# Optimization experiments

Hardware: AMD Instinct MI355X
Metric: run time of the kernel (lower is better)

The kernel has to match this reference:

```python
import jax, jax.numpy as jnp
import numpy as np

T, B, I, H, NC = 1024, 256, 128, 64, 10


def _lstm_cell(x_t, h, c, W_ih, W_hh, b):
    # PyTorch gate order: i, f, g, o. gates: [B, 4H]
    gates = x_t @ W_ih.T + h @ W_hh.T + b
    i, f, g, o = jnp.split(gates, 4, axis=-1)
    i = jax.nn.sigmoid(i)
    f = jax.nn.sigmoid(f)
    g = jnp.tanh(g)
    o = jax.nn.sigmoid(o)
    c = f * c + i * g
    h = o * jnp.tanh(c)
    return h, c


def setup_inputs() -> dict:
    key = jax.random.key(0)
    ks = jax.random.split(key, 12)
    s = 1.0 / np.sqrt(H)  # PyTorch LSTM init scale
    d = {
        "x": jax.random.normal(ks[0], (T, B, I), dtype=jnp.float32),
        # forward direction LSTM params
        "W_ih_f": jax.random.uniform(ks[1], (4 * H, I), minval=-s, maxval=s, dtype=jnp.float32),
        "W_hh_f": jax.random.uniform(ks[2], (4 * H, H), minval=-s, maxval=s, dtype=jnp.float32),
        "b_f": jax.random.uniform(ks[3], (4 * H,), minval=-s, maxval=s, dtype=jnp.float32),
        # reverse direction LSTM params
        "W_ih_r": jax.random.uniform(ks[4], (4 * H, I), minval=-s, maxval=s, dtype=jnp.float32),
        "W_hh_r": jax.random.uniform(ks[5], (4 * H, H), minval=-s, maxval=s, dtype=jnp.float32),
        "b_r": jax.random.uniform(ks[6], (4 * H,), minval=-s, maxval=s, dtype=jnp.float32),
        # MLP head: 2H -> 64 -> 32 -> NC
        "fc1_w": jax.random.normal(ks[7], (64, 2 * H), dtype=jnp.float32) * 0.05,
        "fc1_b": jnp.zeros((64,), dtype=jnp.float32),
        "fc2_w": jax.random.normal(ks[8], (32, 64), dtype=jnp.float32) * 0.05,
        "fc2_b": jnp.zeros((32,), dtype=jnp.float32),
        "fc3_w": jax.random.normal(ks[9], (NC, 32), dtype=jnp.float32) * 0.05,
        "fc3_b": jnp.zeros((NC,), dtype=jnp.float32),
    }
    return d


def _forward(x, W_ih_f, W_hh_f, b_f, W_ih_r, W_hh_r, b_r,
             fc1_w, fc1_b, fc2_w, fc2_b, fc3_w, fc3_b):
    Bsz = x.shape[1]
    h0 = jnp.zeros((Bsz, H), dtype=x.dtype)
    c0 = jnp.zeros((Bsz, H), dtype=x.dtype)

    # Forward direction: only the final hidden state is needed (output[-1] fwd half).
    def fwd_step(carry, x_t):
        h, c = carry
        h, c = _lstm_cell(x_t, h, c, W_ih_f, W_hh_f, b_f)
        return (h, c), None

    (h_fwd_last, _), _ = jax.lax.scan(fwd_step, (h0, c0), x)

    # Reverse direction: output[-1] reverse half is the hidden after processing
    # x[-1] first (reverse scan starts from the last timestep with zero state).
    h_bwd_last, _ = _lstm_cell(x[-1], h0, c0, W_ih_r, W_hh_r, b_r)

    h_cat = jnp.concatenate([h_fwd_last, h_bwd_last], axis=-1)  # [B, 2H]

    h1 = jax.nn.relu(h_cat @ fc1_w.T + fc1_b)
    h2 = jax.nn.relu(h1 @ fc2_w.T + fc2_b)
    out = h2 @ fc3_w.T + fc3_b  # [B, NC]
    return out


def reference(x, W_ih_f, W_hh_f, b_f, W_ih_r, W_hh_r, b_r,
              fc1_w, fc1_b, fc2_w, fc2_b, fc3_w, fc3_b):
    return _forward(x, W_ih_f, W_hh_f, b_f, W_ih_r, W_hh_r, b_r,
                    fc1_w, fc1_b, fc2_w, fc2_b, fc3_w, fc3_b)
```

## Files before the change

kernel.cpp:

```cpp
#include <hip/hip_runtime.h>
#include <math.h>

#define T_LEN 1024
#define B_SZ  256
#define I_SZ  128
#define H_SZ  64
#define G_SZ  256
#define SUB   32

typedef float f32x8 __attribute__((ext_vector_type(8)));

__device__ __forceinline__ float fast_tanh(float x) {
    float e = __expf(-2.0f * fabsf(x));
    float r = (1.0f - e) * __builtin_amdgcn_rcpf(1.0f + e);
    return copysignf(r, x);
}

#define LD8PIN(V, P)                                                        \
    {   float4 t0_ = *reinterpret_cast<const float4*>(P);                   \
        float4 t1_ = *reinterpret_cast<const float4*>((P) + 4);             \
        V = (f32x8){t0_.x, t0_.y, t0_.z, t0_.w, t1_.x, t1_.y, t1_.z, t1_.w};\
        asm volatile("" : "+v"(V)); }

#define RL8(V, K)                                                           \
    {   unsigned r0_ = __builtin_amdgcn_readlane(hu, (K) + 0);              \
        unsigned r1_ = __builtin_amdgcn_readlane(hu, (K) + 1);              \
        unsigned r2_ = __builtin_amdgcn_readlane(hu, (K) + 2);              \
        unsigned r3_ = __builtin_amdgcn_readlane(hu, (K) + 3);              \
        a0 = fmaf(__uint_as_float(r0_), V[0], a0);                          \
        a1 = fmaf(__uint_as_float(r1_), V[1], a1);                          \
        a2 = fmaf(__uint_as_float(r2_), V[2], a2);                          \
        a3 = fmaf(__uint_as_float(r3_), V[3], a3);                          \
        unsigned r4_ = __builtin_amdgcn_readlane(hu, (K) + 4);              \
        unsigned r5_ = __builtin_amdgcn_readlane(hu, (K) + 5);              \
        unsigned r6_ = __builtin_amdgcn_readlane(hu, (K) + 6);              \
        unsigned r7_ = __builtin_amdgcn_readlane(hu, (K) + 7);              \
        a0 = fmaf(__uint_as_float(r4_), V[4], a0);                          \
        a1 = fmaf(__uint_as_float(r5_), V[5], a1);                          \
        a2 = fmaf(__uint_as_float(r6_), V[6], a2);                          \
        a3 = fmaf(__uint_as_float(r7_), V[7], a3); }

__device__ __forceinline__ int swz(int c) { return c + 4 * (c >> 5); }

#define GLOAD(K0)                                                           \
    { _Pragma("unroll") for (int i_ = 0; i_ < 4; ++i_) {                    \
        const int mr_ = srow + 32 * i_;                                     \
        pa[i_] = *reinterpret_cast<const float4*>(                          \
            &xch[(size_t)(mt * 128 + mr_) * I_SZ + (K0) + skk]);            \
        pb[i_] = *reinterpret_cast<const float4*>(                          \
            &W_ih[(size_t)(nt * 128 + mr_) * I_SZ + (K0) + skk]); } }

#define SWRITE(BUF)                                                         \
    { _Pragma("unroll") for (int i_ = 0; i_ < 4; ++i_) {                    \
        const int mr_ = srow + 32 * i_; const int sm_ = swz(mr_);           \
        as[BUF][skk + 0][sm_] = pa[i_].x; as[BUF][skk + 1][sm_] = pa[i_].y; \
        as[BUF][skk + 2][sm_] = pa[i_].z; as[BUF][skk + 3][sm_] = pa[i_].w; \
        bs[BUF][skk + 0][sm_] = pb[i_].x; bs[BUF][skk + 1][sm_] = pb[i_].y; \
        bs[BUF][skk + 2][sm_] = pb[i_].z; bs[BUF][skk + 3][sm_] = pb[i_].w; } }

__global__ __launch_bounds__(256, 2) void xg_gemm(
    const float* __restrict__ xch,
    const float* __restrict__ W_ih,
    const float* __restrict__ bias,
    float* __restrict__ XG)
{
    const int tid = threadIdx.x;
    const int tx  = tid & 15;
    const int ty  = tid >> 4;
    const int mt  = blockIdx.x;
    const int nt  = blockIdx.y;

    __shared__ __align__(16) float as[2][32][140];
    __shared__ __align__(16) float bs[2][32][140];

    const int n0 = nt * 128 + tx * 8;
    float4 bia = *reinterpret_cast<const float4*>(&bias[n0]);
    float4 bib = *reinterpret_cast<const float4*>(&bias[n0 + 4]);

    float acc[8][8];
#pragma unroll
    for (int r = 0; r < 8; ++r)
#pragma unroll
        for (int cc = 0; cc < 8; ++cc) acc[r][cc] = 0.0f;

    const int srow = tid >> 3;
    const int skk  = (tid & 7) * 4;

    float4 pa[4], pb[4];
    GLOAD(0) SWRITE(0)
    __syncthreads();

#pragma unroll
    for (int ks = 0; ks < 4; ++ks) {
        if (ks < 3) GLOAD((ks + 1) * 32)

        const int buf = ks & 1;
#pragma unroll 8
        for (int kk = 0; kk < 32; ++kk) {
            const float4 a0 = *reinterpret_cast<const float4*>(&as[buf][kk][swz(ty * 8)]);
            const float4 a1 = *reinterpret_cast<const float4*>(&as[buf][kk][swz(ty * 8) + 4]);
            const float4 b0 = *reinterpret_cast<const float4*>(&bs[buf][kk][swz(tx * 8)]);
            const float4 b1 = *reinterpret_cast<const float4*>(&bs[buf][kk][swz(tx * 8) + 4]);
            const float av[8] = {a0.x, a0.y, a0.z, a0.w, a1.x, a1.y, a1.z, a1.w};
            const float bv[8] = {b0.x, b0.y, b0.z, b0.w, b1.x, b1.y, b1.z, b1.w};
#pragma unroll
            for (int r = 0; r < 8; ++r)
#pragma unroll
                for (int cc = 0; cc < 8; ++cc)
                    acc[r][cc] = fmaf(av[r], bv[cc], acc[r][cc]);
        }

        if (ks < 3) {
            SWRITE(buf ^ 1)
            __syncthreads();
        }
    }

#pragma unroll
    for (int r = 0; r < 8; ++r) {
        const size_t m = (size_t)(mt * 128 + ty * 8 + r);
        float4 o0 = {acc[r][0] + bia.x, acc[r][1] + bia.y,
                     acc[r][2] + bia.z, acc[r][3] + bia.w};
        float4 o1 = {acc[r][4] + bib.x, acc[r][5] + bib.y,
                     acc[r][6] + bib.z, acc[r][7] + bib.w};
        *reinterpret_cast<float4*>(&XG[m * G_SZ + n0])     = o0;
        *reinterpret_cast<float4*>(&XG[m * G_SZ + n0 + 4]) = o1;
    }
}

__global__ __launch_bounds__(256, 1) void lstm_rec(
    const float* __restrict__ XG,
    const float* __restrict__ W_hh,
    float* __restrict__ h_state,
    float* __restrict__ c_state,
    int TC, int first)
{
    const int b = blockIdx.x;
    const int t = threadIdx.x;
    const int l = t & 63;
    const int g = t >> 6;
    const int row = t;

    __shared__ __align__(16) float xgl[2][SUB][G_SZ];
    __shared__ float gs[2][G_SZ];

    const float* ur = W_hh + row * H_SZ;
    f32x8 w0, w1, w2, w3, w4, w5, w6, w7;
    LD8PIN(w0, ur)      LD8PIN(w1, ur +  8) LD8PIN(w2, ur + 16) LD8PIN(w3, ur + 24)
    LD8PIN(w4, ur + 32) LD8PIN(w5, ur + 40) LD8PIN(w6, ur + 48) LD8PIN(w7, ur + 56)

    float h = first ? 0.0f : h_state[b * H_SZ + l];
    float c = first ? 0.0f : c_state[b * H_SZ + l];

    {
        float* xf = &xgl[0][0][0];
#pragma unroll
        for (int i = 0; i < 8; ++i) {
            const int F = t + 256 * i;
            const int r = F >> 6, cw = F & 63;
            *reinterpret_cast<float4*>(xf + 4 * F) =
                *reinterpret_cast<const float4*>(
                    XG + ((size_t)r * B_SZ + b) * G_SZ + 4 * cw);
        }
    }
    __syncthreads();

    const bool isg = (g == 2);
    const int nsub = TC / SUB;
    int db = 0;

    for (int sub = 0; sub < nsub; ++sub) {
        const int cur = sub & 1;
        if (sub + 1 < nsub) {
            float* xf = &xgl[cur ^ 1][0][0];
#pragma unroll
            for (int i = 0; i < 8; ++i) {
                const int F = t + 256 * i;
                const int r = (F >> 6) + (sub + 1) * SUB, cw = F & 63;
                *reinterpret_cast<float4*>(xf + 4 * F) =
                    *reinterpret_cast<const float4*>(
                        XG + ((size_t)r * B_SZ + b) * G_SZ + 4 * cw);
            }
        }

#pragma unroll 4
        for (int ts = 0; ts < SUB; ++ts) {
            const unsigned hu = __float_as_uint(h);
            float a0 = xgl[cur][ts][row];
            float a1 = 0.0f, a2 = 0.0f, a3 = 0.0f;
            RL8(w0,  0) RL8(w1,  8) RL8(w2, 16) RL8(w3, 24)
            RL8(w4, 32) RL8(w5, 40) RL8(w6, 48) RL8(w7, 56)
            const float acc = (a0 + a1) + (a2 + a3);

            const float arg = isg ? (-2.0f * acc) : (-acc);
            const float e = __expf(arg);
            const float r = __builtin_amdgcn_rcpf(1.0f + e);
            const float a = isg ? (1.0f - e) * r : r;

            gs[db][row] = a;
            __syncthreads();

            const float ig = gs[db][l];
            const float fg = gs[db][H_SZ + l];
            const float gg = gs[db][2 * H_SZ + l];
            const float og = gs[db][3 * H_SZ + l];
            c = fmaf(fg, c, ig * gg);
            h = og * fast_tanh(c);
            db ^= 1;
        }
    }

    if (t < H_SZ) {
        h_state[b * H_SZ + t] = h;
        c_state[b * H_SZ + t] = c;
    }
}

__global__ __launch_bounds__(256, 1) void lstm_tail(
    const float* __restrict__ x_last,
    const float* __restrict__ W_ih_r,
    const float* __restrict__ b_r,
    const float* __restrict__ h_fwd,
    const float* __restrict__ fc1_w,
    const float* __restrict__ fc1_b,
    const float* __restrict__ fc2_w,
    const float* __restrict__ fc2_b,
    const float* __restrict__ fc3_w,
    const float* __restrict__ fc3_b,
    float* __restrict__ out)
{
    const int b = blockIdx.x;
    const int j = threadIdx.x;

    __shared__ float xs[I_SZ];
    __shared__ float gs[G_SZ];
    __shared__ float hc[2 * H_SZ];
    __shared__ float h1[64];
    __shared__ float h2[32];

    if (j < I_SZ) xs[j] = x_last[(size_t)b * I_SZ + j];
    if (j < H_SZ) hc[j] = h_fwd[b * H_SZ + j];
    __syncthreads();

    float a0 = b_r[j], a1 = 0.0f, a2 = 0.0f, a3 = 0.0f;
    const float* wrow = W_ih_r + j * I_SZ;
#pragma unroll
    for (int kk = 0; kk < I_SZ; kk += 4) {
        float4 wv = *reinterpret_cast<const float4*>(wrow + kk);
        a0 = fmaf(xs[kk + 0], wv.x, a0);
        a1 = fmaf(xs[kk + 1], wv.y, a1);
        a2 = fmaf(xs[kk + 2], wv.z, a2);
        a3 = fmaf(xs[kk + 3], wv.w, a3);
    }
    const float acc = (a0 + a1) + (a2 + a3);
    const int gate = j >> 6;
    gs[j] = (gate == 2) ? tanhf(acc) : 1.0f / (1.0f + expf(-acc));
    __syncthreads();

    if (j < H_SZ) {
        const float cc = gs[j] * gs[2 * H_SZ + j];
        hc[H_SZ + j] = gs[3 * H_SZ + j] * tanhf(cc);
    }
    __syncthreads();

    if (j < 64) {
        float s0 = fc1_b[j], s1 = 0.0f, s2 = 0.0f, s3 = 0.0f;
        const float* w = fc1_w + j * 128;
#pragma unroll
        for (int kk = 0; kk < 128; kk += 4) {
            float4 wv = *reinterpret_cast<const float4*>(w + kk);
            s0 = fmaf(hc[kk + 0], wv.x, s0);
            s1 = fmaf(hc[kk + 1], wv.y, s1);
            s2 = fmaf(hc[kk + 2], wv.z, s2);
            s3 = fmaf(hc[kk + 3], wv.w, s3);
        }
        h1[j] = fmaxf((s0 + s1) + (s2 + s3), 0.0f);
    }
    __syncthreads();

    if (j < 32) {
        float s0 = fc2_b[j], s1 = 0.0f, s2 = 0.0f, s3 = 0.0f;
        const float* w = fc2_w + j * 64;
#pragma unroll
        for (int kk = 0; kk < 64; kk += 4) {
            float4 wv = *reinterpret_cast<const float4*>(w + kk);
            s0 = fmaf(h1[kk + 0], wv.x, s0);
            s1 = fmaf(h1[kk + 1], wv.y, s1);
            s2 = fmaf(h1[kk + 2], wv.z, s2);
            s3 = fmaf(h1[kk + 3], wv.w, s3);
        }
        h2[j] = fmaxf((s0 + s1) + (s2 + s3), 0.0f);
    }
    __syncthreads();

    if (j < 10) {
        float s = fc3_b[j];
#pragma unroll
        for (int kk = 0; kk < 32; ++kk) s = fmaf(h2[kk], fc3_w[j * 32 + kk], s);
        out[b * 10 + j] = s;
    }
}

extern "C" void kernel_launch(void* const* d_in, const int* in_sizes, int n_in,
                              void* d_out, int out_size, void* d_ws, size_t ws_size,
                              hipStream_t stream) {
    const float* x      = (const float*)d_in[0];
    const float* W_ih_f = (const float*)d_in[1];
    const float* W_hh_f = (const float*)d_in[2];
    const float* b_f    = (const float*)d_in[3];
    const float* W_ih_r = (const float*)d_in[4];
    const float* b_r    = (const float*)d_in[6];
    const float* fc1_w  = (const float*)d_in[7];
    const float* fc1_b  = (const float*)d_in[8];
    const float* fc2_w  = (const float*)d_in[9];
    const float* fc2_b  = (const float*)d_in[10];
    const float* fc3_w  = (const float*)d_in[11];
    const float* fc3_b  = (const float*)d_in[12];
    float* out = (float*)d_out;

    int TC = 1024;
    while (TC > 64 &&
           (size_t)TC * B_SZ * G_SZ * 4 + 2 * B_SZ * H_SZ * 4 > ws_size)
        TC >>= 1;

    float* XG      = (float*)d_ws;
    float* h_state = (float*)((char*)d_ws + (size_t)TC * B_SZ * G_SZ * 4);
    float* c_state = h_state + B_SZ * H_SZ;

    const int NCH = T_LEN / TC;
    for (int ch = 0; ch < NCH; ++ch) {
        const float* xch = x + (size_t)ch * TC * B_SZ * I_SZ;
        hipLaunchKernelGGL(xg_gemm, dim3(TC * B_SZ / 128, 2), dim3(256), 0,
                           stream, xch, W_ih_f, b_f, XG);
        hipLaunchKernelGGL(lstm_rec, dim3(B_SZ), dim3(256), 0, stream,
                           XG, W_hh_f, h_state, c_state, TC, ch == 0 ? 1 : 0);
    }

    const float* x_last = x + (size_t)(T_LEN - 1) * B_SZ * I_SZ;
    hipLaunchKernelGGL(lstm_tail, dim3(B_SZ), dim3(256), 0, stream,
                       x_last, W_ih_r, b_r, h_state,
                       fc1_w, fc1_b, fc2_w, fc2_b, fc3_w, fc3_b, out);
}
```

Baseline: 607.2 us.

## Pack two batch rows per recurrence block with 512 threads

The recurrent LSTM kernel now processes two batch elements per workgroup: 512 threads, with each half owning its own slice of shared memory. The grid shrinks to half as many blocks. The sub-chunk length is halved so the doubled staging buffers fit in the same LDS footprint. The aim is to interleave two independent recurrences on one CU so each can hide the other's latency. The cost is that the per-step barrier now spans eight waves, and only half as many CUs are occupied.

```diff
diff --git a/kernel.cpp b/kernel.cpp
--- a/kernel.cpp
+++ b/kernel.cpp
@@ -6,7 +6,7 @@
 #define I_SZ  128
 #define H_SZ  64
 #define G_SZ  256
-#define SUB   32
+#define SUB   16
 
 typedef float f32x8 __attribute__((ext_vector_type(8)));
 
@@ -128,21 +128,23 @@
     }
 }
 
-__global__ __launch_bounds__(256, 1) void lstm_rec(
+__global__ __launch_bounds__(512, 1) void lstm_rec(
     const float* __restrict__ XG,
     const float* __restrict__ W_hh,
     float* __restrict__ h_state,
     float* __restrict__ c_state,
     int TC, int first)
 {
-    const int b = blockIdx.x;
-    const int t = threadIdx.x;
-    const int l = t & 63;
-    const int g = t >> 6;
-    const int row = t;
-
-    __shared__ __align__(16) float xgl[2][SUB][G_SZ];
-    __shared__ float gs[2][G_SZ];
+    const int t   = threadIdx.x;
+    const int bb  = t >> 8;
+    const int tt  = t & 255;
+    const int b   = blockIdx.x * 2 + bb;
+    const int l   = tt & 63;
+    const int g   = tt >> 6;
+    const int row = tt;
+
+    __shared__ __align__(16) float xgl[2][2][SUB][G_SZ];
+    __shared__ float gs[2][2][G_SZ];
 
     const float* ur = W_hh + row * H_SZ;
     f32x8 w0, w1, w2, w3, w4, w5, w6, w7;
@@ -153,10 +155,10 @@
     float c = first ? 0.0f : c_state[b * H_SZ + l];
 
     {
-        float* xf = &xgl[0][0][0];
-#pragma unroll
-        for (int i = 0; i < 8; ++i) {
-            const int F = t + 256 * i;
+        float* xf = &xgl[bb][0][0][0];
+#pragma unroll
+        for (int i = 0; i < 4; ++i) {
+            const int F = tt + 256 * i;
             const int r = F >> 6, cw = F & 63;
             *reinterpret_cast<float4*>(xf + 4 * F) =
                 *reinterpret_cast<const float4*>(
@@ -172,10 +174,10 @@
     for (int sub = 0; sub < nsub; ++sub) {
         const int cur = sub & 1;
         if (sub + 1 < nsub) {
-            float* xf = &xgl[cur ^ 1][0][0];
-#pragma unroll
-            for (int i = 0; i < 8; ++i) {
-                const int F = t + 256 * i;
+            float* xf = &xgl[bb][cur ^ 1][0][0];
+#pragma unroll
+            for (int i = 0; i < 4; ++i) {
+                const int F = tt + 256 * i;
                 const int r = (F >> 6) + (sub + 1) * SUB, cw = F & 63;
                 *reinterpret_cast<float4*>(xf + 4 * F) =
                     *reinterpret_cast<const float4*>(
@@ -186,7 +188,7 @@
 #pragma unroll 4
         for (int ts = 0; ts < SUB; ++ts) {
             const unsigned hu = __float_as_uint(h);
-            float a0 = xgl[cur][ts][row];
+            float a0 = xgl[bb][cur][ts][row];
             float a1 = 0.0f, a2 = 0.0f, a3 = 0.0f;
             RL8(w0,  0) RL8(w1,  8) RL8(w2, 16) RL8(w3, 24)
             RL8(w4, 32) RL8(w5, 40) RL8(w6, 48) RL8(w7, 56)
@@ -197,22 +199,22 @@
             const float r = __builtin_amdgcn_rcpf(1.0f + e);
             const float a = isg ? (1.0f - e) * r : r;
 
-            gs[db][row] = a;
+            gs[bb][db][row] = a;
             __syncthreads();
 
-            const float ig = gs[db][l];
-            const float fg = gs[db][H_SZ + l];
-            const float gg = gs[db][2 * H_SZ + l];
-            const float og = gs[db][3 * H_SZ + l];
+            const float ig = gs[bb][db][l];
+            const float fg = gs[bb][db][H_SZ + l];
+            const float gg = gs[bb][db][2 * H_SZ + l];
+            const float og = gs[bb][db][3 * H_SZ + l];
             c = fmaf(fg, c, ig * gg);
             h = og * fast_tanh(c);
             db ^= 1;
         }
     }
 
-    if (t < H_SZ) {
-        h_state[b * H_SZ + t] = h;
-        c_state[b * H_SZ + t] = c;
+    if (tt < H_SZ) {
+        h_state[b * H_SZ + tt] = h;
+        c_state[b * H_SZ + tt] = c;
     }
 }
 
@@ -332,7 +334,7 @@
         const float* xch = x + (size_t)ch * TC * B_SZ * I_SZ;
         hipLaunchKernelGGL(xg_gemm, dim3(TC * B_SZ / 128, 2), dim3(256), 0,
                            stream, xch, W_ih_f, b_f, XG);
-        hipLaunchKernelGGL(lstm_rec, dim3(B_SZ), dim3(256), 0, stream,
+        hipLaunchKernelGGL(lstm_rec, dim3(B_SZ / 2), dim3(512), 0, stream,
                            XG, W_hh_f, h_state, c_state, TC, ch == 0 ? 1 : 0);
     }
 
```

Measured after the change: 819.7 us. +35.0%, slower.

## Run LSTM recurrence in a single wavefront per batch row without barriers

Applied to the files above, without the earlier changes.

The recurrent kernel now uses one 64-lane wavefront per batch element. Each lane holds all four gate rows of W_hh in registers (256 floats) and computes all four gates itself. This removes the shared-memory gate exchange and the per-timestep __syncthreads. The next timestep's input gates are prefetched straight from global memory instead of staged chunks in LDS. In exchange, register pressure rises sharply, risking spills. Each step now does four times the readlane/FMA work serially on one wave, with far fewer waves per CU.

```diff
diff --git a/kernel.cpp b/kernel.cpp
--- a/kernel.cpp
+++ b/kernel.cpp
@@ -6,10 +6,17 @@
 #define I_SZ  128
 #define H_SZ  64
 #define G_SZ  256
-#define SUB   32
 
 typedef float f32x8 __attribute__((ext_vector_type(8)));
 
+__device__ __forceinline__ float fast_sigmoid(float x) {
+    float e = __expf(-x);
+    return __builtin_amdgcn_rcpf(1.0f + e);
+}
+__device__ __forceinline__ float fast_tanh_b(float x) {
+    float e = __expf(-2.0f * x);
+    return (1.0f - e) * __builtin_amdgcn_rcpf(1.0f + e);
+}
 __device__ __forceinline__ float fast_tanh(float x) {
     float e = __expf(-2.0f * fabsf(x));
     float r = (1.0f - e) * __builtin_amdgcn_rcpf(1.0f + e);
@@ -22,23 +29,14 @@
         V = (f32x8){t0_.x, t0_.y, t0_.z, t0_.w, t1_.x, t1_.y, t1_.z, t1_.w};\
         asm volatile("" : "+v"(V)); }
 
-#define RL8(V, K)                                                           \
-    {   unsigned r0_ = __builtin_amdgcn_readlane(hu, (K) + 0);              \
-        unsigned r1_ = __builtin_amdgcn_readlane(hu, (K) + 1);              \
-        unsigned r2_ = __builtin_amdgcn_readlane(hu, (K) + 2);              \
-        unsigned r3_ = __builtin_amdgcn_readlane(hu, (K) + 3);              \
-        a0 = fmaf(__uint_as_float(r0_), V[0], a0);                          \
-        a1 = fmaf(__uint_as_float(r1_), V[1], a1);                          \
-        a2 = fmaf(__uint_as_float(r2_), V[2], a2);                          \
-        a3 = fmaf(__uint_as_float(r3_), V[3], a3);                          \
-        unsigned r4_ = __builtin_amdgcn_readlane(hu, (K) + 4);              \
-        unsigned r5_ = __builtin_amdgcn_readlane(hu, (K) + 5);              \
-        unsigned r6_ = __builtin_amdgcn_readlane(hu, (K) + 6);              \
-        unsigned r7_ = __builtin_amdgcn_readlane(hu, (K) + 7);              \
-        a0 = fmaf(__uint_as_float(r4_), V[4], a0);                          \
-        a1 = fmaf(__uint_as_float(r5_), V[5], a1);                          \
-        a2 = fmaf(__uint_as_float(r6_), V[6], a2);                          \
-        a3 = fmaf(__uint_as_float(r7_), V[7], a3); }
+#define DOT8(VI, VF, VG, VO, K)                                             \
+    { _Pragma("unroll") for (int q_ = 0; q_ < 8; ++q_) {                    \
+        unsigned s_ = __builtin_amdgcn_readlane(hu, (K) + q_);              \
+        const float hv_ = __uint_as_float(s_);                              \
+        ai = fmaf(hv_, VI[q_], ai);                                         \
+        af = fmaf(hv_, VF[q_], af);                                         \
+        ag = fmaf(hv_, VG[q_], ag);                                         \
+        ao = fmaf(hv_, VO[q_], ao); } }
 
 __device__ __forceinline__ int swz(int c) { return c + 4 * (c >> 5); }
 
@@ -128,7 +126,7 @@
     }
 }
 
-__global__ __launch_bounds__(256, 1) void lstm_rec(
+__global__ __launch_bounds__(64, 1) void lstm_rec(
     const float* __restrict__ XG,
     const float* __restrict__ W_hh,
     float* __restrict__ h_state,
@@ -136,84 +134,60 @@
     int TC, int first)
 {
     const int b = blockIdx.x;
-    const int t = threadIdx.x;
-    const int l = t & 63;
-    const int g = t >> 6;
-    const int row = t;
-
-    __shared__ __align__(16) float xgl[2][SUB][G_SZ];
-    __shared__ float gs[2][G_SZ];
-
-    const float* ur = W_hh + row * H_SZ;
-    f32x8 w0, w1, w2, w3, w4, w5, w6, w7;
-    LD8PIN(w0, ur)      LD8PIN(w1, ur +  8) LD8PIN(w2, ur + 16) LD8PIN(w3, ur + 24)
-    LD8PIN(w4, ur + 32) LD8PIN(w5, ur + 40) LD8PIN(w6, ur + 48) LD8PIN(w7, ur + 56)
+    const int l = threadIdx.x;
+
+    const float* ri = W_hh + (0 * H_SZ + l) * H_SZ;
+    const float* rf = W_hh + (1 * H_SZ + l) * H_SZ;
+    const float* rg = W_hh + (2 * H_SZ + l) * H_SZ;
+    const float* ro = W_hh + (3 * H_SZ + l) * H_SZ;
+    f32x8 wi0, wi1, wi2, wi3, wi4, wi5, wi6, wi7;
+    f32x8 wf0, wf1, wf2, wf3, wf4, wf5, wf6, wf7;
+    f32x8 wg0, wg1, wg2, wg3, wg4, wg5, wg6, wg7;
+    f32x8 wo0, wo1, wo2, wo3, wo4, wo5, wo6, wo7;
+    LD8PIN(wi0, ri)      LD8PIN(wi1, ri +  8) LD8PIN(wi2, ri + 16) LD8PIN(wi3, ri + 24)
+    LD8PIN(wi4, ri + 32) LD8PIN(wi5, ri + 40) LD8PIN(wi6, ri + 48) LD8PIN(wi7, ri + 56)
+    LD8PIN(wf0, rf)      LD8PIN(wf1, rf +  8) LD8PIN(wf2, rf + 16) LD8PIN(wf3, rf + 24)
+    LD8PIN(wf4, rf + 32) LD8PIN(wf5, rf + 40) LD8PIN(wf6, rf + 48) LD8PIN(wf7, rf + 56)
+    LD8PIN(wg0, rg)      LD8PIN(wg1, rg +  8) LD8PIN(wg2, rg + 16) LD8PIN(wg3, rg + 24)
+    LD8PIN(wg4, rg + 32) LD8PIN(wg5, rg + 40) LD8PIN(wg6, rg + 48) LD8PIN(wg7, rg + 56)
+    LD8PIN(wo0, ro)      LD8PIN(wo1, ro +  8) LD8PIN(wo2, ro + 16) LD8PIN(wo3, ro + 24)
+    LD8PIN(wo4, ro + 32) LD8PIN(wo5, ro + 40) LD8PIN(wo6, ro + 48) LD8PIN(wo7, ro + 56)
 
     float h = first ? 0.0f : h_state[b * H_SZ + l];
     float c = first ? 0.0f : c_state[b * H_SZ + l];
 
-    {
-        float* xf = &xgl[0][0][0];
-#pragma unroll
-        for (int i = 0; i < 8; ++i) {
-            const int F = t + 256 * i;
-            const int r = F >> 6, cw = F & 63;
-            *reinterpret_cast<float4*>(xf + 4 * F) =
-                *reinterpret_cast<const float4*>(
-                    XG + ((size_t)r * B_SZ + b) * G_SZ + 4 * cw);
-        }
-    }
-    __syncthreads();
-
-    const bool isg = (g == 2);
-    const int nsub = TC / SUB;
-    int db = 0;
-
-    for (int sub = 0; sub < nsub; ++sub) {
-        const int cur = sub & 1;
-        if (sub + 1 < nsub) {
-            float* xf = &xgl[cur ^ 1][0][0];
-#pragma unroll
-            for (int i = 0; i < 8; ++i) {
-                const int F = t + 256 * i;
-                const int r = (F >> 6) + (sub + 1) * SUB, cw = F & 63;
-                *reinterpret_cast<float4*>(xf + 4 * F) =
-                    *reinterpret_cast<const float4*>(
-                        XG + ((size_t)r * B_SZ + b) * G_SZ + 4 * cw);
-            }
-        }
-
-#pragma unroll 4
-        for (int ts = 0; ts < SUB; ++ts) {
-            const unsigned hu = __float_as_uint(h);
-            float a0 = xgl[cur][ts][row];
-            float a1 = 0.0f, a2 = 0.0f, a3 = 0.0f;
-            RL8(w0,  0) RL8(w1,  8) RL8(w2, 16) RL8(w3, 24)
-            RL8(w4, 32) RL8(w5, 40) RL8(w6, 48) RL8(w7, 56)
-            const float acc = (a0 + a1) + (a2 + a3);
-
-            const float arg = isg ? (-2.0f * acc) : (-acc);
-            const float e = __expf(arg);
-            const float r = __builtin_amdgcn_rcpf(1.0f + e);
-            const float a = isg ? (1.0f - e) * r : r;
-
-            gs[db][row] = a;
-            __syncthreads();
-
-            const float ig = gs[db][l];
-            const float fg = gs[db][H_SZ + l];
-            const float gg = gs[db][2 * H_SZ + l];
-            const float og = gs[db][3 * H_SZ + l];
-            c = fmaf(fg, c, ig * gg);
-            h = og * fast_tanh(c);
-            db ^= 1;
-        }
-    }
-
-    if (t < H_SZ) {
-        h_state[b * H_SZ + t] = h;
-        c_state[b * H_SZ + t] = c;
-    }
+    const float* xgp = XG + (size_t)b * G_SZ;
+    const size_t tstride = (size_t)B_SZ * G_SZ;
+
+    float xi = xgp[l], xf = xgp[H_SZ + l], xg = xgp[2 * H_SZ + l], xo = xgp[3 * H_SZ + l];
+
+    for (int t = 0; t < TC; ++t) {
+        float ni = 0.0f, nf = 0.0f, ng = 0.0f, no = 0.0f;
+        if (t + 1 < TC) {
+            const float* p = xgp + (size_t)(t + 1) * tstride;
+            ni = p[l]; nf = p[H_SZ + l]; ng = p[2 * H_SZ + l]; no = p[3 * H_SZ + l];
+        }
+
+        const unsigned hu = __float_as_uint(h);
+        float ai = xi, af = xf, ag = xg, ao = xo;
+        DOT8(wi0, wf0, wg0, wo0,  0) DOT8(wi1, wf1, wg1, wo1,  8)
+        DOT8(wi2, wf2, wg2, wo2, 16) DOT8(wi3, wf3, wg3, wo3, 24)
+        DOT8(wi4, wf4, wg4, wo4, 32) DOT8(wi5, wf5, wg5, wo5, 40)
+        DOT8(wi6, wf6, wg6, wo6, 48) DOT8(wi7, wf7, wg7, wo7, 56)
+
+        const float i_ = fast_sigmoid(ai);
+        const float f_ = fast_sigmoid(af);
+        const float g_ = fast_tanh_b(ag);
+        const float o_ = fast_sigmoid(ao);
+
+        c = fmaf(f_, c, i_ * g_);
+        h = o_ * fast_tanh(c);
+
+        xi = ni; xf = nf; xg = ng; xo = no;
+    }
+
+    h_state[b * H_SZ + l] = h;
+    c_state[b * H_SZ + l] = c;
 }
 
 __global__ __launch_bounds__(256, 1) void lstm_tail(
@@ -332,7 +306,7 @@
         const float* xch = x + (size_t)ch * TC * B_SZ * I_SZ;
         hipLaunchKernelGGL(xg_gemm, dim3(TC * B_SZ / 128, 2), dim3(256), 0,
                            stream, xch, W_ih_f, b_f, XG);
-        hipLaunchKernelGGL(lstm_rec, dim3(B_SZ), dim3(256), 0, stream,
+        hipLaunchKernelGGL(lstm_rec, dim3(B_SZ), dim3(64), 0, stream,
                            XG, W_hh_f, h_state, c_state, TC, ch == 0 ? 1 : 0);
     }
 
```

Result: slower. 1.501 ms (+147.3%).
